# Optimization experiments

Hardware: AMD Instinct MI355X
Metric: run time of the kernel (lower is better)

Reference implementation:

```python
import jax, jax.numpy as jnp
import numpy as np

B, M, FIN = 16, 49152, 16
F1, K = 32, 5
NNZ = 8 * M  # ~8 neighbors per vertex on a HEALPix sphere mesh


def setup_inputs() -> dict:
    key = jax.random.key(0)
    kx, kr, kc, kv, kw, kb = jax.random.split(key, 6)
    x = jax.random.normal(kx, (B, M, FIN), dtype=jnp.float32)
    rows = jax.random.randint(kr, (NNZ,), 0, M, dtype=jnp.int32)
    cols = jax.random.randint(kc, (NNZ,), 0, M, dtype=jnp.int32)
    # small values keep the order-K Chebyshev recurrence numerically tame
    vals = jax.random.normal(kv, (NNZ,), dtype=jnp.float32) * 0.1
    stddev = 1.0 / np.sqrt(FIN * (K + 0.5) / 2.0)
    kernel = jax.random.normal(kw, (FIN * K, F1), dtype=jnp.float32) * stddev
    bias = jax.random.uniform(kb, (1, 1, F1), dtype=jnp.float32) * 0.05
    return {"x": x, "rows": rows, "cols": cols, "vals": vals,
            "kernel": kernel, "bias": bias}


def reference(x, rows, cols, vals, kernel, bias):
    # x: [B, M, Fin]; sparse Laplacian L in COO (rows, cols, vals), shape [M, M]
    b, m, fin = x.shape
    k = kernel.shape[0] // fin

    def spmm(X):  # L @ X for X: [M, Fin*B]
        return jax.ops.segment_sum(vals[:, None] * X[cols], rows, num_segments=m)

    # x0: [M, Fin*B] exactly as the TF transpose/reshape does
    x0 = jnp.transpose(x, (1, 2, 0)).reshape(m, fin * b)
    xs = [x0]
    if k > 1:
        x1 = spmm(x0)
        xs.append(x1)
    for _ in range(2, k):
        x2 = 2.0 * spmm(x1) - x0
        xs.append(x2)
        x0, x1 = x1, x2
    # [K, M, Fin, B] -> [B, M, Fin, K] -> [B*M, Fin*K]
    xk = jnp.stack(xs, axis=0).reshape(k, m, fin, b)
    xk = jnp.transpose(xk, (3, 1, 2, 0)).reshape(b * m, fin * k)
    out = (xk @ kernel).reshape(b, m, -1)  # [B, M, F1]
    return out + bias
```

## Files before the change

### kernel.cpp

```cpp
#include <hip/hip_runtime.h>


constexpr int M   = 49152;
constexpr int B   = 16;
constexpr int FIN = 16;
constexpr int F1  = 32;
constexpr int K   = 5;
constexpr int FB  = B * FIN;
constexpr int RW  = FB / 4;
constexpr int XBS = M * FIN;

typedef short s16x8 __attribute__((ext_vector_type(8)));
typedef float f32x4 __attribute__((ext_vector_type(4)));

#define DEVFN __device__ __forceinline__

DEVFN float bf2f(unsigned short h) {
  union { unsigned int u; float f; } v;
  v.u = (unsigned int)h << 16;
  return v.f;
}
DEVFN unsigned short f2bf(float f) {
  union { float f; unsigned int u; } v;
  v.f = f;
  unsigned int r = (v.u + 0x7FFFu + ((v.u >> 16) & 1u)) >> 16;
  return (unsigned short)r;
}
DEVFN float4 bf4(ushort4 u) {
  return make_float4(bf2f(u.x), bf2f(u.y), bf2f(u.z), bf2f(u.w));
}


__global__ __launch_bounds__(256) void transform_x(const float* __restrict__ x,
                                                   ushort4* __restrict__ x0b) {
  int lane = threadIdx.x & 63;
  int m = blockIdx.x * 4 + (threadIdx.x >> 6);
  int b = lane >> 2, f0 = (lane & 3) * 4;
  float4 v = *(const float4*)(x + (size_t)b * XBS + (size_t)m * FIN + f0);
  x0b[(size_t)m * RW + lane] = make_ushort4(f2bf(v.x), f2bf(v.y), f2bf(v.z), f2bf(v.w));
}


__global__ __launch_bounds__(256) void hist_kernel(const int* __restrict__ rows,
                                                   int* __restrict__ counts, int nnz) {
  int i = blockIdx.x * 256 + threadIdx.x;
  if (i < nnz) atomicAdd(&counts[rows[i]], 1);
}

DEVFN int wave_incl_scan(int v, int lane) {
#pragma unroll
  for (int off = 1; off < 64; off <<= 1) {
    int t = __shfl_up(v, off);
    if (lane >= off) v += t;
  }
  return v;
}

__global__ __launch_bounds__(1024) void scan_blocks(const int* __restrict__ counts,
                                                    int* __restrict__ row_ptr,
                                                    int* __restrict__ partials) {
  __shared__ int wsum[16];
  int tid = threadIdx.x, lane = tid & 63, w = tid >> 6;
  int i = blockIdx.x * 1024 + tid;
  int s = wave_incl_scan(counts[i], lane);
  if (lane == 63) wsum[w] = s;
  __syncthreads();
  if (tid < 16) {
    int t = wsum[tid];
#pragma unroll
    for (int off = 1; off < 16; off <<= 1) {
      int u = __shfl_up(t, off);
      if (tid >= off) t += u;
    }
    wsum[tid] = t;
  }
  __syncthreads();
  int base = (w > 0) ? wsum[w - 1] : 0;
  s += base;
  row_ptr[i + 1] = s;
  if (tid == 1023) partials[blockIdx.x] = s;
}

__global__ void scan_partials_kernel(int* __restrict__ partials,
                                     int* __restrict__ row_ptr, int nblk) {
  int lane = threadIdx.x;
  int v = (lane < nblk) ? partials[lane] : 0;
  v = wave_incl_scan(v, lane);
  if (lane < nblk) partials[lane] = v;
  if (lane == 0) row_ptr[0] = 0;
}

__global__ __launch_bounds__(1024) void scan_add_kernel(int* __restrict__ row_ptr,
                                                        const int* __restrict__ partials) {
  if (blockIdx.x == 0) return;
  int i = blockIdx.x * 1024 + threadIdx.x;
  row_ptr[i + 1] += partials[blockIdx.x - 1];
}

__global__ __launch_bounds__(256) void scatter_kernel(const int* __restrict__ rows,
                                                      const int* __restrict__ cols,
                                                      const float* __restrict__ vals,
                                                      const int* __restrict__ row_ptr,
                                                      int* __restrict__ fill,
                                                      int2* __restrict__ cv, int nnz) {
  int i = blockIdx.x * 256 + threadIdx.x;
  if (i < nnz) {
    int r = rows[i];
    int pos = row_ptr[r] + atomicAdd(&fill[r], 1);
    cv[pos] = make_int2(cols[i], __float_as_int(vals[i]));
  }
}


template <bool SUB>
__global__ __launch_bounds__(256) void spmm_bf16(const ushort4* __restrict__ gsrc,
                                                 const ushort4* __restrict__ ssrc,
                                                 ushort4* __restrict__ y,
                                                 const int* __restrict__ row_ptr,
                                                 const int2* __restrict__ cv) {
  int lane = threadIdx.x & 63;
  int m = blockIdx.x * 4 + (threadIdx.x >> 6);
  int beg = row_ptr[m], end = row_ptr[m + 1];
  float a0 = 0.f, a1 = 0.f, a2 = 0.f, a3 = 0.f;
  int e = beg;
  for (; e + 2 <= end; e += 2) {
    int2 p0 = cv[e];
    int2 p1 = cv[e + 1];
    ushort4 xv0 = gsrc[(size_t)p0.x * RW + lane];
    ushort4 xv1 = gsrc[(size_t)p1.x * RW + lane];
    float v0 = __int_as_float(p0.y);
    float v1 = __int_as_float(p1.y);
    a0 = fmaf(v0, bf2f(xv0.x), a0);
    a1 = fmaf(v0, bf2f(xv0.y), a1);
    a2 = fmaf(v0, bf2f(xv0.z), a2);
    a3 = fmaf(v0, bf2f(xv0.w), a3);
    a0 = fmaf(v1, bf2f(xv1.x), a0);
    a1 = fmaf(v1, bf2f(xv1.y), a1);
    a2 = fmaf(v1, bf2f(xv1.z), a2);
    a3 = fmaf(v1, bf2f(xv1.w), a3);
  }
  if (e < end) {
    int2 p = cv[e];
    float v = __int_as_float(p.y);
    ushort4 xv = gsrc[(size_t)p.x * RW + lane];
    a0 = fmaf(v, bf2f(xv.x), a0);
    a1 = fmaf(v, bf2f(xv.y), a1);
    a2 = fmaf(v, bf2f(xv.z), a2);
    a3 = fmaf(v, bf2f(xv.w), a3);
  }
  if (SUB) {
    float4 s = bf4(ssrc[(size_t)m * RW + lane]);
    a0 = fmaf(2.f, a0, -s.x);
    a1 = fmaf(2.f, a1, -s.y);
    a2 = fmaf(2.f, a2, -s.z);
    a3 = fmaf(2.f, a3, -s.w);
  }
  y[(size_t)m * RW + lane] = make_ushort4(f2bf(a0), f2bf(a1), f2bf(a2), f2bf(a3));
}


__global__ __launch_bounds__(256) void cheb_gemm_mfma(const ushort4* __restrict__ xs0,
                                                      const float* __restrict__ kern,
                                                      const float* __restrict__ bias,
                                                      float* __restrict__ out) {
  __shared__ unsigned short bl[3][4][32][8];
  __shared__ float bsl[32];
  int tid = threadIdx.x;
  for (int idx = tid; idx < 3 * 4 * 32 * 8; idx += 256) {
    int j = idx & 7, o = (idx >> 3) & 31, g = (idx >> 8) & 3, c = idx >> 10;
    int k = 2 * c + (g >> 1), f = (g & 1) * 8 + j;
    bl[c][g][o][j] = (k < K) ? f2bf(kern[(f * K + k) * F1 + o]) : (unsigned short)0;
  }
  if (tid < 32) bsl[tid] = bias[tid];
  __syncthreads();

  int lane = tid & 63;
  int w = blockIdx.x * 4 + (tid >> 6);
  int b = w / 384;
  int mt0 = (w % 384) * 8;

  int row = lane & 15, g = lane >> 4;
  int col = lane & 15;

  s16x8 bf[3][2];
#pragma unroll
  for (int c = 0; c < 3; ++c) {
#pragma unroll
    for (int ot = 0; ot < 2; ++ot)
      bf[c][ot] = *(const s16x8*)(&bl[c][g][col + 16 * ot][0]);
  }
  float bias0 = bsl[col], bias1 = bsl[col + 16];

  const char* xsbase = (const char*)xs0;
  const size_t BUFBYTES = (size_t)M * 512;
  size_t lanebyte = (size_t)row * 512 + (size_t)b * 32 + (size_t)(g & 1) * 16;
  int khalf = g >> 1;
  const char* p0 = xsbase + (size_t)(0 + khalf) * BUFBYTES + lanebyte;
  const char* p1 = xsbase + (size_t)(2 + khalf) * BUFBYTES + lanebyte;
  const char* p2 = xsbase + (size_t)(4 + khalf) * BUFBYTES + lanebyte;

  size_t obase0 = ((size_t)b * M + (size_t)mt0 * 16) * F1;

#pragma unroll 2
  for (int t = 0; t < 8; ++t) {
    size_t moff = (size_t)(mt0 + t) * (16 * 512);
    s16x8 a0 = *(const s16x8*)(p0 + moff);
    s16x8 a1 = *(const s16x8*)(p1 + moff);
    s16x8 a2 = (g < 2) ? *(const s16x8*)(p2 + moff) : (s16x8)0;

    f32x4 acc0 = {0.f, 0.f, 0.f, 0.f};
    f32x4 acc1 = {0.f, 0.f, 0.f, 0.f};
    acc0 = __builtin_amdgcn_mfma_f32_16x16x32_bf16(a0, bf[0][0], acc0, 0, 0, 0);
    acc1 = __builtin_amdgcn_mfma_f32_16x16x32_bf16(a0, bf[0][1], acc1, 0, 0, 0);
    acc0 = __builtin_amdgcn_mfma_f32_16x16x32_bf16(a1, bf[1][0], acc0, 0, 0, 0);
    acc1 = __builtin_amdgcn_mfma_f32_16x16x32_bf16(a1, bf[1][1], acc1, 0, 0, 0);
    acc0 = __builtin_amdgcn_mfma_f32_16x16x32_bf16(a2, bf[2][0], acc0, 0, 0, 0);
    acc1 = __builtin_amdgcn_mfma_f32_16x16x32_bf16(a2, bf[2][1], acc1, 0, 0, 0);

    float* ob = out + obase0 + (size_t)t * (16 * F1);
#pragma unroll
    for (int j = 0; j < 4; ++j) {
      int r = g * 4 + j;
      ob[r * F1 + col]      = acc0[j] + bias0;
      ob[r * F1 + col + 16] = acc1[j] + bias1;
    }
  }
}


extern "C" void kernel_launch(void* const* d_in, const int* in_sizes, int n_in,
                              void* d_out, int out_size, void* d_ws, size_t ws_size,
                              hipStream_t stream) {
  const float* x    = (const float*)d_in[0];
  const int*   rows = (const int*)d_in[1];
  const int*   cols = (const int*)d_in[2];
  const float* vals = (const float*)d_in[3];
  const float* kern = (const float*)d_in[4];
  const float* bias = (const float*)d_in[5];
  float* out = (float*)d_out;
  int nnz = in_sizes[1];

  const size_t BUF = (size_t)M * RW;
  ushort4* x0b = (ushort4*)d_ws;
  ushort4* x1b = x0b + BUF;
  ushort4* x2b = x1b + BUF;
  ushort4* x3b = x2b + BUF;
  ushort4* x4b = x3b + BUF;
  int* row_ptr  = (int*)(x4b + BUF);
  int* counts   = row_ptr + (M + 256);
  int* fill     = counts + M;
  int* partials = fill + M;
  int2* cv      = (int2*)(partials + 256);

  int nblk1024 = M / 1024;
  int nblkNnz  = (nnz + 255) / 256;

  transform_x<<<M / 4, 256, 0, stream>>>(x, x0b);

  hipMemsetAsync(counts, 0, (size_t)2 * M * 4, stream);
  hist_kernel<<<nblkNnz, 256, 0, stream>>>(rows, counts, nnz);
  scan_blocks<<<nblk1024, 1024, 0, stream>>>(counts, row_ptr, partials);
  scan_partials_kernel<<<1, 64, 0, stream>>>(partials, row_ptr, nblk1024);
  scan_add_kernel<<<nblk1024, 1024, 0, stream>>>(row_ptr, partials);
  scatter_kernel<<<nblkNnz, 256, 0, stream>>>(rows, cols, vals, row_ptr, fill, cv, nnz);

  spmm_bf16<false><<<M / 4, 256, 0, stream>>>(x0b, nullptr, x1b, row_ptr, cv);
  spmm_bf16<true ><<<M / 4, 256, 0, stream>>>(x1b, x0b, x2b, row_ptr, cv);
  spmm_bf16<true ><<<M / 4, 256, 0, stream>>>(x2b, x1b, x3b, row_ptr, cv);
  spmm_bf16<true ><<<M / 4, 256, 0, stream>>>(x3b, x2b, x4b, row_ptr, cv);

  cheb_gemm_mfma<<<1536, 256, 0, stream>>>(x0b, kern, bias, out);

  (void)n_in; (void)out_size; (void)ws_size; (void)in_sizes;
}
```

Baseline: 274.5 us.

## Split feature buffers into batch slices for cache-resident SpMM gathers

```diff
diff --git a/kernel.cpp b/kernel.cpp
--- a/kernel.cpp
+++ b/kernel.cpp
@@ -7,8 +7,9 @@
 constexpr int F1  = 32;
 constexpr int K   = 5;
 constexpr int FB  = B * FIN;
-constexpr int RW  = FB / 4;
 constexpr int XBS = M * FIN;
+constexpr size_t SLICEB   = (size_t)M * 64;
+constexpr size_t BUFBYTES = (size_t)M * 512;
 
 typedef short s16x8 __attribute__((ext_vector_type(8)));
 typedef float f32x4 __attribute__((ext_vector_type(4)));
@@ -19,6 +20,12 @@
   union { unsigned int u; float f; } v;
   v.u = (unsigned int)h << 16;
   return v.f;
+}
+DEVFN float lo2f(unsigned int d) {
+  union { unsigned int u; float f; } v; v.u = d << 16; return v.f;
+}
+DEVFN float hi2f(unsigned int d) {
+  union { unsigned int u; float f; } v; v.u = d & 0xffff0000u; return v.f;
 }
 DEVFN unsigned short f2bf(float f) {
   union { float f; unsigned int u; } v;
@@ -26,18 +33,17 @@
   unsigned int r = (v.u + 0x7FFFu + ((v.u >> 16) & 1u)) >> 16;
   return (unsigned short)r;
 }
-DEVFN float4 bf4(ushort4 u) {
-  return make_float4(bf2f(u.x), bf2f(u.y), bf2f(u.z), bf2f(u.w));
-}
 
 
 __global__ __launch_bounds__(256) void transform_x(const float* __restrict__ x,
-                                                   ushort4* __restrict__ x0b) {
+                                                   char* __restrict__ x0b) {
   int lane = threadIdx.x & 63;
   int m = blockIdx.x * 4 + (threadIdx.x >> 6);
-  int b = lane >> 2, f0 = (lane & 3) * 4;
-  float4 v = *(const float4*)(x + (size_t)b * XBS + (size_t)m * FIN + f0);
-  x0b[(size_t)m * RW + lane] = make_ushort4(f2bf(v.x), f2bf(v.y), f2bf(v.z), f2bf(v.w));
+  int s = lane >> 3, i = lane & 7;
+  int b = 2 * s + (i >> 2), f = (i & 3) * 4;
+  float4 v = *(const float4*)(x + (size_t)b * XBS + (size_t)m * FIN + f);
+  ushort4 r = make_ushort4(f2bf(v.x), f2bf(v.y), f2bf(v.z), f2bf(v.w));
+  *(ushort4*)(x0b + (size_t)s * SLICEB + (size_t)m * 64 + i * 8) = r;
 }
 
 
@@ -113,53 +119,54 @@
 
 
 template <bool SUB>
-__global__ __launch_bounds__(256) void spmm_bf16(const ushort4* __restrict__ gsrc,
-                                                 const ushort4* __restrict__ ssrc,
-                                                 ushort4* __restrict__ y,
-                                                 const int* __restrict__ row_ptr,
-                                                 const int2* __restrict__ cv) {
-  int lane = threadIdx.x & 63;
-  int m = blockIdx.x * 4 + (threadIdx.x >> 6);
-  int beg = row_ptr[m], end = row_ptr[m + 1];
-  float a0 = 0.f, a1 = 0.f, a2 = 0.f, a3 = 0.f;
-  int e = beg;
-  for (; e + 2 <= end; e += 2) {
-    int2 p0 = cv[e];
-    int2 p1 = cv[e + 1];
-    ushort4 xv0 = gsrc[(size_t)p0.x * RW + lane];
-    ushort4 xv1 = gsrc[(size_t)p1.x * RW + lane];
-    float v0 = __int_as_float(p0.y);
-    float v1 = __int_as_float(p1.y);
-    a0 = fmaf(v0, bf2f(xv0.x), a0);
-    a1 = fmaf(v0, bf2f(xv0.y), a1);
-    a2 = fmaf(v0, bf2f(xv0.z), a2);
-    a3 = fmaf(v0, bf2f(xv0.w), a3);
-    a0 = fmaf(v1, bf2f(xv1.x), a0);
-    a1 = fmaf(v1, bf2f(xv1.y), a1);
-    a2 = fmaf(v1, bf2f(xv1.z), a2);
-    a3 = fmaf(v1, bf2f(xv1.w), a3);
-  }
-  if (e < end) {
-    int2 p = cv[e];
-    float v = __int_as_float(p.y);
-    ushort4 xv = gsrc[(size_t)p.x * RW + lane];
-    a0 = fmaf(v, bf2f(xv.x), a0);
-    a1 = fmaf(v, bf2f(xv.y), a1);
-    a2 = fmaf(v, bf2f(xv.z), a2);
-    a3 = fmaf(v, bf2f(xv.w), a3);
-  }
-  if (SUB) {
-    float4 s = bf4(ssrc[(size_t)m * RW + lane]);
-    a0 = fmaf(2.f, a0, -s.x);
-    a1 = fmaf(2.f, a1, -s.y);
-    a2 = fmaf(2.f, a2, -s.z);
-    a3 = fmaf(2.f, a3, -s.w);
-  }
-  y[(size_t)m * RW + lane] = make_ushort4(f2bf(a0), f2bf(a1), f2bf(a2), f2bf(a3));
-}
-
-
-__global__ __launch_bounds__(256) void cheb_gemm_mfma(const ushort4* __restrict__ xs0,
+__global__ __launch_bounds__(256) void spmm_slice(const char* __restrict__ xsrc,
+                                                  const char* __restrict__ ssrc,
+                                                  char* __restrict__ y,
+                                                  const int* __restrict__ row_ptr,
+                                                  const int2* __restrict__ cv) {
+  int s  = blockIdx.x & 7;
+  int rg = blockIdx.x >> 3;
+  int lane = threadIdx.x & 63, wave = threadIdx.x >> 6;
+  int grp = lane >> 4, fl = lane & 15;
+  int fl4 = fl * 4;
+  const char* sbase = xsrc + (size_t)s * SLICEB;
+  const char* subbase = ssrc + (size_t)s * SLICEB;
+  char* ybase = y + (size_t)s * SLICEB;
+  int m0 = rg * 64 + wave * 16;
+
+  for (int mi = 0; mi < 16; ++mi) {
+    int m = m0 + mi;
+    int beg = row_ptr[m], end = row_ptr[m + 1];
+    int nt4 = (end - beg + 3) >> 2;
+    float a0 = 0.f, a1 = 0.f;
+    int e = beg + grp;
+    for (int t = 0; t < nt4; ++t, e += 4) {
+      if (e < end) {
+        long long ll = __builtin_nontemporal_load((const long long*)(cv + e));
+        int c = (int)ll;
+        float v = __int_as_float((int)(ll >> 32));
+        unsigned int d = *(const unsigned int*)(sbase + (size_t)c * 64 + fl4);
+        a0 = fmaf(v, lo2f(d), a0);
+        a1 = fmaf(v, hi2f(d), a1);
+      }
+    }
+    a0 += __shfl_xor(a0, 16); a0 += __shfl_xor(a0, 32);
+    a1 += __shfl_xor(a1, 16); a1 += __shfl_xor(a1, 32);
+    if (grp == 0) {
+      if (SUB) {
+        unsigned int sv = __builtin_nontemporal_load(
+            (const unsigned int*)(subbase + (size_t)m * 64 + fl4));
+        a0 = fmaf(2.f, a0, -lo2f(sv));
+        a1 = fmaf(2.f, a1, -hi2f(sv));
+      }
+      unsigned int r = ((unsigned int)f2bf(a1) << 16) | (unsigned int)f2bf(a0);
+      __builtin_nontemporal_store(r, (unsigned int*)(ybase + (size_t)m * 64 + fl4));
+    }
+  }
+}
+
+
+__global__ __launch_bounds__(256) void cheb_gemm_mfma(const char* __restrict__ xs0,
                                                       const float* __restrict__ kern,
                                                       const float* __restrict__ bias,
                                                       float* __restrict__ out) {
@@ -191,19 +198,18 @@
   }
   float bias0 = bsl[col], bias1 = bsl[col + 16];
 
-  const char* xsbase = (const char*)xs0;
-  const size_t BUFBYTES = (size_t)M * 512;
-  size_t lanebyte = (size_t)row * 512 + (size_t)b * 32 + (size_t)(g & 1) * 16;
+  size_t lanebyte = (size_t)(b >> 1) * SLICEB + (size_t)row * 64 +
+                    (size_t)(b & 1) * 32 + (size_t)(g & 1) * 16;
   int khalf = g >> 1;
-  const char* p0 = xsbase + (size_t)(0 + khalf) * BUFBYTES + lanebyte;
-  const char* p1 = xsbase + (size_t)(2 + khalf) * BUFBYTES + lanebyte;
-  const char* p2 = xsbase + (size_t)(4 + khalf) * BUFBYTES + lanebyte;
+  const char* p0 = xs0 + (size_t)(0 + khalf) * BUFBYTES + lanebyte;
+  const char* p1 = xs0 + (size_t)(2 + khalf) * BUFBYTES + lanebyte;
+  const char* p2 = xs0 + (size_t)(4 + khalf) * BUFBYTES + lanebyte;
 
   size_t obase0 = ((size_t)b * M + (size_t)mt0 * 16) * F1;
 
 #pragma unroll 2
   for (int t = 0; t < 8; ++t) {
-    size_t moff = (size_t)(mt0 + t) * (16 * 512);
+    size_t moff = (size_t)(mt0 + t) * (16 * 64);
     s16x8 a0 = *(const s16x8*)(p0 + moff);
     s16x8 a1 = *(const s16x8*)(p1 + moff);
     s16x8 a2 = (g < 2) ? *(const s16x8*)(p2 + moff) : (s16x8)0;
@@ -221,8 +227,8 @@
 #pragma unroll
     for (int j = 0; j < 4; ++j) {
       int r = g * 4 + j;
-      ob[r * F1 + col]      = acc0[j] + bias0;
-      ob[r * F1 + col + 16] = acc1[j] + bias1;
+      __builtin_nontemporal_store(acc0[j] + bias0, ob + r * F1 + col);
+      __builtin_nontemporal_store(acc1[j] + bias1, ob + r * F1 + col + 16);
     }
   }
 }
@@ -240,13 +246,12 @@
   float* out = (float*)d_out;
   int nnz = in_sizes[1];
 
-  const size_t BUF = (size_t)M * RW;
-  ushort4* x0b = (ushort4*)d_ws;
-  ushort4* x1b = x0b + BUF;
-  ushort4* x2b = x1b + BUF;
-  ushort4* x3b = x2b + BUF;
-  ushort4* x4b = x3b + BUF;
-  int* row_ptr  = (int*)(x4b + BUF);
+  char* x0b = (char*)d_ws;
+  char* x1b = x0b + BUFBYTES;
+  char* x2b = x1b + BUFBYTES;
+  char* x3b = x2b + BUFBYTES;
+  char* x4b = x3b + BUFBYTES;
+  int* row_ptr  = (int*)(x4b + BUFBYTES);
   int* counts   = row_ptr + (M + 256);
   int* fill     = counts + M;
   int* partials = fill + M;
@@ -264,10 +269,11 @@
   scan_add_kernel<<<nblk1024, 1024, 0, stream>>>(row_ptr, partials);
   scatter_kernel<<<nblkNnz, 256, 0, stream>>>(rows, cols, vals, row_ptr, fill, cv, nnz);
 
-  spmm_bf16<false><<<M / 4, 256, 0, stream>>>(x0b, nullptr, x1b, row_ptr, cv);
-  spmm_bf16<true ><<<M / 4, 256, 0, stream>>>(x1b, x0b, x2b, row_ptr, cv);
-  spmm_bf16<true ><<<M / 4, 256, 0, stream>>>(x2b, x1b, x3b, row_ptr, cv);
-  spmm_bf16<true ><<<M / 4, 256, 0, stream>>>(x3b, x2b, x4b, row_ptr, cv);
+  int spmmGrid = 8 * (M / 64);
+  spmm_slice<false><<<spmmGrid, 256, 0, stream>>>(x0b, nullptr, x1b, row_ptr, cv);
+  spmm_slice<true ><<<spmmGrid, 256, 0, stream>>>(x1b, x0b, x2b, row_ptr, cv);
+  spmm_slice<true ><<<spmmGrid, 256, 0, stream>>>(x2b, x1b, x3b, row_ptr, cv);
+  spmm_slice<true ><<<spmmGrid, 256, 0, stream>>>(x3b, x2b, x4b, row_ptr, cv);
 
   cheb_gemm_mfma<<<1536, 256, 0, stream>>>(x0b, kern, bias, out);
 
```

New measurement: 761.8 us. +177.5%, slower.
